# Optimization experiments

Measured on AMD Instinct MI355X. Metric: run time of the kernel, lower is better.

## Reference

```python
import jax, jax.numpy as jnp
import numpy as np

B, S, HOPS, DIM, NREL = 1024, 32, 2, 64, 237
NENT, NEDGE = 14541, 272115
SIGMA = 0.1
CFMW = 64


def setup_inputs() -> dict:
    key = jax.random.key(0)
    ks = jax.random.split(key, 20)

    def g(k, shape):
        return (jax.random.normal(k, shape, dtype=jnp.float32) / np.float32(np.sqrt(shape[0])))

    inp = {
        "entity_pairs": jax.random.randint(ks[0], (B, 2), 0, NENT),
        "train_edges": jax.random.randint(ks[1], (B,), 0, NEDGE),
        "labels": jax.random.randint(ks[2], (B,), 0, NREL),
        "entity2edges": jax.random.randint(ks[3], (NENT + 1, S), 0, NEDGE + 1),
        "edge2entities": jax.random.randint(ks[4], (NEDGE + 1, 1), 0, NENT + 1),
        "edge2relation": jax.random.randint(ks[5], (NEDGE + 1,), 0, NREL + 1),
        "t": jax.random.uniform(ks[6], (B,), dtype=jnp.float32),
        "eps": jax.random.normal(ks[7], (B, NREL), dtype=jnp.float32),
        "rel_feat": g(ks[8], (NREL, DIM)),
        "W_agg0": g(ks[9], (DIM, DIM)), "b_agg0": jnp.zeros((DIM,), jnp.float32),
        "W_agg1": g(ks[10], (DIM, NREL)), "b_agg1": jnp.zeros((NREL,), jnp.float32),
        "W_out": g(ks[11], (2 * NREL, NREL)), "b_out": jnp.zeros((NREL,), jnp.float32),
        "mW1": g(ks[12], (NREL + 1, CFMW)), "mb1": jnp.zeros((CFMW,), jnp.float32),
        "mW2": g(ks[13], (CFMW, CFMW)), "mb2": jnp.zeros((CFMW,), jnp.float32),
        "mW3": g(ks[14], (CFMW, CFMW)), "mb3": jnp.zeros((CFMW,), jnp.float32),
        "mW4": g(ks[15], (CFMW, NREL)), "mb4": jnp.zeros((NREL,), jnp.float32),
    }
    return inp


def _side(ent, labels, train_edges, entity2edges, edge2entities, edge2relation, relf, aggs):
    # multi-hop neighbor edge gather + masks (exclude the training edge itself)
    edges_list = [labels]  # hop-0 "edges" are the relation labels
    masks = []
    for i in range(HOPS):
        if i == 0:
            ne = ent.reshape(B, 1)  # (B, 1) source entities
        else:
            ne = edge2entities[edges_list[-1].reshape(-1)].reshape(B, -1)
        nedges = entity2edges[ne.reshape(-1)].reshape(B, -1)  # (B, S**(i+1))
        edges_list.append(nedges)
        masks.append((nedges != train_edges[:, None]).astype(relf.dtype))
    # edge -> relation -> feature
    ev = [relf[edges_list[0]]]  # (B, DIM)
    for edges in edges_list[1:]:
        ev.append(relf[edge2relation[edges]])  # (B, S**h, DIM)
    # iterative mean aggregation (PathCon-style, one entity per edge)
    for i in range(HOPS):
        W, b, act, self_inc = aggs[i]
        d = W.shape[0]
        nxt = []
        for hop in range(HOPS - i):
            neigh = ev[hop + 1].reshape(B, -1, 1, S, d)
            m = masks[hop].reshape(B, -1, 1, S, 1)
            out = jnp.mean(jnp.mean(neigh * m, axis=-2), axis=-2)  # (B, S**hop, d)
            if self_inc:
                out = out + ev[hop].reshape(B, -1, d)
            nxt.append(act(out @ W + b))
        ev = nxt
    return ev[0].reshape(B, NREL)


def reference(entity_pairs, train_edges, labels, entity2edges, edge2entities,
              edge2relation, t, eps, rel_feat, W_agg0, b_agg0, W_agg1, b_agg1,
              W_out, b_out, mW1, mb1, mW2, mb2, mW3, mb3, mW4, mb4):
    relf = jnp.concatenate([rel_feat, jnp.zeros((1, DIM), rel_feat.dtype)], axis=0)
    aggs = [
        (W_agg0, b_agg0, jax.nn.relu, True),    # intermediate hop: relu, self-included
        (W_agg1, b_agg1, lambda x: x, False),   # last hop: identity, no self
    ]
    x0 = _side(entity_pairs[:, 0], labels, train_edges, entity2edges,
               edge2entities, edge2relation, relf, aggs)
    x1 = _side(entity_pairs[:, 1], labels, train_edges, entity2edges,
               edge2entities, edge2relation, relf, aggs)
    output = jnp.concatenate([x0, x1], axis=-1) @ W_out + b_out  # (B, NREL)
    # CFM: xt = (1-t) x0 + t x1 + sigma*eps ; ut = x1 - x0
    tb = t[:, None]
    xt = (1.0 - tb) * x0 + tb * x1 + SIGMA * eps
    h = jnp.concatenate([xt, tb], axis=-1)
    h = jax.nn.selu(h @ mW1 + mb1)
    h = jax.nn.selu(h @ mW2 + mb2)
    h = jax.nn.selu(h @ mW3 + mb3)
    vt = h @ mW4 + mb4
    scores = output * vt
    return scores
```

## Files before the change

### kernel.cpp

```cpp
#include <hip/hip_runtime.h>
#include <math.h>

#define BB 1024
#define S 32
#define DIM 64
#define NREL 237
#define SIGMA 0.1f

#define OFS_WR    0
#define N_WR      (238*64)
#define OFS_OVEC  (OFS_WR + N_WR)
#define N_OVEC    (2048*64)
#define OFS_WC0   (OFS_OVEC + N_OVEC)
#define N_WC      (64*237)
#define OFS_WC1   (OFS_WC0 + N_WC)
#define OFS_M1    (OFS_WC1 + N_WC)
#define N_M1      (64*64)
#define OFS_BC    (OFS_M1 + N_M1)
#define OFS_HC    (OFS_BC + 237)

__device__ __forceinline__ float selu_f(float x) {
    const float alpha = 1.6732632423543772f;
    const float scale = 1.0507009873554805f;
    return scale * (x > 0.f ? x : alpha * expm1f(x));
}

__global__ __launch_bounds__(256) void precompute_kernel(
    const float* __restrict__ rel_feat, const float* __restrict__ W0,
    const float* __restrict__ W1, const float* __restrict__ b1,
    const float* __restrict__ W_out, const float* __restrict__ b_out,
    const float* __restrict__ mW1, const float* __restrict__ mb1,
    float* __restrict__ ws) {
    __shared__ float red[256];
    int blk = blockIdx.x;
    const int tid = threadIdx.x;

    if (blk < 60) {
        int idx = blk * 256 + tid;
        if (idx < 238 * 64) {
            int r = idx >> 6, o = idx & 63;
            float acc = 0.f;
            if (r < NREL) {
#pragma unroll 8
                for (int d = 0; d < 64; ++d)
                    acc += rel_feat[r * 64 + d] * W0[d * 64 + o];
            }
            ws[OFS_WR + idx] = acc;
        }
        return;
    }
    blk -= 60;
    if (blk < 512) {
        int half = blk >> 8;
        int lb = blk & 255;
        int o = lb >> 2, ct = lb & 3;
        int cl = tid & 63, g = tid >> 6;
        int c = ct * 64 + cl;
        const float* Wsrc = W_out + half * 237 * 237;
        float acc = 0.f;
        if (c < NREL) {
            int k0 = g * 60, k1 = (g == 3) ? 237 : (k0 + 60);
#pragma unroll 4
            for (int k = k0; k < k1; ++k)
                acc += W1[o * 237 + k] * Wsrc[k * 237 + c];
        }
        red[tid] = acc;
        __syncthreads();
        if (g == 0 && c < NREL) {
            float s = red[cl] + red[64 + cl] + red[128 + cl] + red[192 + cl];
            ws[(half ? OFS_WC1 : OFS_WC0) + o * 237 + c] = s;
        }
        return;
    }
    blk -= 512;
    if (blk < 64) {
        int o = blk;
        int w = tid & 63, g = tid >> 6;
        int k0 = g * 60, k1 = (g == 3) ? 237 : (k0 + 60);
        float acc = 0.f;
#pragma unroll 4
        for (int k = k0; k < k1; ++k)
            acc += W1[o * 237 + k] * mW1[k * 64 + w];
        red[tid] = acc;
        __syncthreads();
        if (g == 0)
            ws[OFS_M1 + o * 64 + w] = red[w] + red[64 + w] + red[128 + w] + red[192 + w];
        return;
    }
    blk -= 64;
    if (blk < 4) {
        int cl = tid & 63, g = tid >> 6;
        int c = blk * 64 + cl;
        float acc = 0.f;
        if (c < NREL) {
            int k0 = g * 60, k1 = (g == 3) ? 237 : (k0 + 60);
#pragma unroll 4
            for (int k = k0; k < k1; ++k)
                acc += b1[k] * (W_out[k * 237 + c] + W_out[(237 + k) * 237 + c]);
        }
        red[tid] = acc;
        __syncthreads();
        if (g == 0 && c < NREL)
            ws[OFS_BC + c] = b_out[c] + red[cl] + red[64 + cl] + red[128 + cl] + red[192 + cl];
        return;
    }
    {
        int w = tid & 63, g = tid >> 6;
        int k0 = g * 60, k1 = (g == 3) ? 237 : (k0 + 60);
        float acc = 0.f;
#pragma unroll 4
        for (int k = k0; k < k1; ++k)
            acc += b1[k] * mW1[k * 64 + w];
        red[tid] = acc;
        __syncthreads();
        if (g == 0)
            ws[OFS_HC + w] = mb1[w] + red[w] + red[64 + w] + red[128 + w] + red[192 + w];
    }
}

__global__ __launch_bounds__(256) void gather_kernel(
    const int* __restrict__ ep, const int* __restrict__ te_arr,
    const int* __restrict__ e2e_tab, const int* __restrict__ e2ent,
    const int* __restrict__ e2r, const float* __restrict__ b0,
    float* __restrict__ ws) {
    extern __shared__ float smem[];
    float* s_wr   = smem;
    int*   s_r2m  = (int*)(smem + 15232);
    int*   s_r1   = (int*)(smem + 16256);
    int*   s_ent2 = (int*)(smem + 16288);
    float* s_m1   = smem + 16320;
    float* s_v1   = smem + 16352;

    const int tid = threadIdx.x;
    const int bbase = blockIdx.x * 2;
    const int g = tid >> 4;
    const int c = tid & 15;
    const float4 b0v = ((const float4*)b0)[c];

    {
        const float4* src = (const float4*)(ws + OFS_WR);
        float4* dst = (float4*)s_wr;
        for (int i = tid; i < 238 * 16; i += 256) dst[i] = src[i];
    }
    const float4* sWr4 = (const float4*)s_wr;

    for (int u = 0; u < 4; ++u) {
        const int b = bbase + (u >> 1);
        const int side = u & 1;
        const int te = te_arr[b];
        if (tid < 32) {
            int ent = ep[b * 2 + side];
            int e1 = e2e_tab[ent * S + tid];
            s_r1[tid] = e2r[e1];
            s_m1[tid] = (e1 != te) ? 1.0f : 0.0f;
            s_ent2[tid] = e2ent[e1];
        }
        __syncthreads();
        for (int p = tid; p < 1024; p += 256) {
            int j = p >> 5, s = p & 31;
            int e2 = e2e_tab[s_ent2[j] * S + s];
            s_r2m[p] = (e2 == te) ? NREL : e2r[e2];
        }
        __syncthreads();
        for (int jj = g; jj < 32; jj += 16) {
            float4 acc = sWr4[s_r1[jj] * 16 + c];
            float4 sa = make_float4(0.f, 0.f, 0.f, 0.f);
            float4 sb = make_float4(0.f, 0.f, 0.f, 0.f);
            const int* rr = &s_r2m[jj * 32];
#pragma unroll
            for (int s = 0; s < 16; ++s) {
                float4 v = sWr4[rr[s] * 16 + c];
                sa.x += v.x; sa.y += v.y; sa.z += v.z; sa.w += v.w;
            }
#pragma unroll
            for (int s = 16; s < 32; ++s) {
                float4 v = sWr4[rr[s] * 16 + c];
                sb.x += v.x; sb.y += v.y; sb.z += v.z; sb.w += v.w;
            }
            const float inv = 1.0f / 32.0f;
            float m = s_m1[jj];
            float4 r;
            r.x = fmaxf(acc.x + (sa.x + sb.x) * inv + b0v.x, 0.f) * m;
            r.y = fmaxf(acc.y + (sa.y + sb.y) * inv + b0v.y, 0.f) * m;
            r.z = fmaxf(acc.z + (sa.z + sb.z) * inv + b0v.z, 0.f) * m;
            r.w = fmaxf(acc.w + (sa.w + sb.w) * inv + b0v.w, 0.f) * m;
            *((float4*)&s_v1[jj * 68 + c * 4]) = r;
        }
        __syncthreads();
        if (tid < 64) {
            float sum = 0.f;
#pragma unroll 8
            for (int j = 0; j < 32; ++j) sum += s_v1[j * 68 + tid];
            ws[OFS_OVEC + (b * 2 + side) * 64 + tid] = sum * (1.0f / 32.0f);
        }
        __syncthreads();
    }
}

__global__ __launch_bounds__(256) void final_kernel(
    const float* __restrict__ t_arr, const float* __restrict__ eps,
    const float* __restrict__ mW1, const float* __restrict__ mW2,
    const float* __restrict__ mb2, const float* __restrict__ mW3,
    const float* __restrict__ mb3, const float* __restrict__ mW4,
    const float* __restrict__ mb4, const float* __restrict__ ws,
    float* __restrict__ out) {
    __shared__ float s_o0[2][64], s_o1[2][64], s_omix[2][64];
    __shared__ float s_out[2][240];
    __shared__ float s_red[2][256];
    __shared__ float s_h[2][64];

    const int tid = threadIdx.x;
    const int bb = blockIdx.x * 2;
    const float* ovec = ws + OFS_OVEC;
    const float* Wc0 = ws + OFS_WC0;
    const float* Wc1 = ws + OFS_WC1;
    const float* M1 = ws + OFS_M1;
    const float* bc = ws + OFS_BC;
    const float* hc = ws + OFS_HC;
    const float tb0 = t_arr[bb];
    const float tb1 = t_arr[bb + 1];

    if (tid < 128) {
        int p = tid >> 6, w = tid & 63;
        float tb = p ? tb1 : tb0;
        float o0 = ovec[((bb + p) * 2 + 0) * 64 + w];
        float o1 = ovec[((bb + p) * 2 + 1) * 64 + w];
        s_o0[p][w] = o0; s_o1[p][w] = o1;
        s_omix[p][w] = (1.f - tb) * o0 + tb * o1;
    }
    __syncthreads();

    if (tid < NREL) {
        float a0 = bc[tid], a1 = a0;
#pragma unroll 4
        for (int d = 0; d < 64; ++d) {
            float w0 = Wc0[d * 237 + tid];
            float w1 = Wc1[d * 237 + tid];
            a0 += s_o0[0][d] * w0 + s_o1[0][d] * w1;
            a1 += s_o0[1][d] * w0 + s_o1[1][d] * w1;
        }
        s_out[0][tid] = a0;
        s_out[1][tid] = a1;
    }

    {
        int w = tid & 63, gg = tid >> 6;
        float a0 = 0.f, a1 = 0.f;
        int k0 = gg * 60, k1 = (gg == 3) ? 237 : (k0 + 60);
        const float* e0 = eps + bb * 237;
        const float* e1 = eps + (bb + 1) * 237;
#pragma unroll 4
        for (int k = k0; k < k1; ++k) {
            float m = mW1[k * 64 + w];
            a0 += e0[k] * m;
            a1 += e1[k] * m;
        }
        a0 *= SIGMA; a1 *= SIGMA;
#pragma unroll
        for (int d = gg * 16; d < gg * 16 + 16; ++d) {
            float m = M1[d * 64 + w];
            a0 += s_omix[0][d] * m;
            a1 += s_omix[1][d] * m;
        }
        s_red[0][tid] = a0;
        s_red[1][tid] = a1;
    }
    __syncthreads();
    if (tid < 128) {
        int p = tid >> 6, w = tid & 63;
        float tb = p ? tb1 : tb0;
        float h = hc[w] + tb * mW1[237 * 64 + w]
                + s_red[p][w] + s_red[p][64 + w] + s_red[p][128 + w] + s_red[p][192 + w];
        s_h[p][w] = selu_f(h);
    }
    __syncthreads();

    {
        int w = tid & 63, gg = tid >> 6;
        float a0 = 0.f, a1 = 0.f;
#pragma unroll
        for (int d = gg * 16; d < gg * 16 + 16; ++d) {
            float m = mW2[d * 64 + w];
            a0 += s_h[0][d] * m;
            a1 += s_h[1][d] * m;
        }
        s_red[0][tid] = a0;
        s_red[1][tid] = a1;
    }
    __syncthreads();
    if (tid < 128) {
        int p = tid >> 6, w = tid & 63;
        s_h[p][w] = 0.f;
        float v = mb2[w] + s_red[p][w] + s_red[p][64 + w] + s_red[p][128 + w] + s_red[p][192 + w];
        s_h[p][w] = selu_f(v);
    }
    __syncthreads();

    {
        int w = tid & 63, gg = tid >> 6;
        float a0 = 0.f, a1 = 0.f;
#pragma unroll
        for (int d = gg * 16; d < gg * 16 + 16; ++d) {
            float m = mW3[d * 64 + w];
            a0 += s_h[0][d] * m;
            a1 += s_h[1][d] * m;
        }
        s_red[0][tid] = a0;
        s_red[1][tid] = a1;
    }
    __syncthreads();
    if (tid < 128) {
        int p = tid >> 6, w = tid & 63;
        float v = mb3[w] + s_red[p][w] + s_red[p][64 + w] + s_red[p][128 + w] + s_red[p][192 + w];
        s_h[p][w] = selu_f(v);
    }
    __syncthreads();

    if (tid < NREL) {
        float a0 = mb4[tid], a1 = a0;
#pragma unroll 4
        for (int w = 0; w < 64; ++w) {
            float m = mW4[w * 237 + tid];
            a0 += s_h[0][w] * m;
            a1 += s_h[1][w] * m;
        }
        out[bb * 237 + tid] = s_out[0][tid] * a0;
        out[(bb + 1) * 237 + tid] = s_out[1][tid] * a1;
    }
}

extern "C" void kernel_launch(void* const* d_in, const int* in_sizes, int n_in,
                              void* d_out, int out_size, void* d_ws, size_t ws_size,
                              hipStream_t stream) {
    const int* ep       = (const int*)d_in[0];
    const int* te       = (const int*)d_in[1];
    const int* e2e      = (const int*)d_in[3];
    const int* e2ent    = (const int*)d_in[4];
    const int* e2r      = (const int*)d_in[5];
    const float* t      = (const float*)d_in[6];
    const float* eps    = (const float*)d_in[7];
    const float* relf   = (const float*)d_in[8];
    const float* W0     = (const float*)d_in[9];
    const float* b0     = (const float*)d_in[10];
    const float* W1     = (const float*)d_in[11];
    const float* b1     = (const float*)d_in[12];
    const float* W_out  = (const float*)d_in[13];
    const float* b_out  = (const float*)d_in[14];
    const float* mW1    = (const float*)d_in[15];
    const float* mb1    = (const float*)d_in[16];
    const float* mW2    = (const float*)d_in[17];
    const float* mb2    = (const float*)d_in[18];
    const float* mW3    = (const float*)d_in[19];
    const float* mb3    = (const float*)d_in[20];
    const float* mW4    = (const float*)d_in[21];
    const float* mb4    = (const float*)d_in[22];
    float* ws  = (float*)d_ws;
    float* out = (float*)d_out;

    hipLaunchKernelGGL(precompute_kernel, dim3(641), dim3(256), 0, stream,
                       relf, W0, W1, b1, W_out, b_out, mW1, mb1, ws);
    hipLaunchKernelGGL(gather_kernel, dim3(BB / 2), dim3(256), 74112, stream,
                       ep, te, e2e, e2ent, e2r, b0, ws);
    hipLaunchKernelGGL(final_kernel, dim3(BB / 2), dim3(256), 0, stream,
                       t, eps, mW1, mW2, mb2, mW3, mb3, mW4, mb4, ws, out);
}
```

Measured before the change: 154.8 us.

## Fuse gather and final MLP kernels; compute W1 projection in-kernel instead of precomputed M1

Merges the gather kernel and the final CFM/MLP kernel into one, so the per-pair aggregated vectors stay in shared memory instead of round-tripping through the workspace, and one launch disappears. The precomputed W1·mW1 product (M1) is dropped. Each block now projects the mixed vector through W1 and folds it into the mW1 matvec alongside the noise term. Hop-1 lookups for all four side/pair units are fetched up front, and the next unit's hop-2 indices are prefetched inside the loop. The cost is a larger shared-memory footprint per block and a somewhat bigger matvec per block.

```diff
diff --git a/kernel.cpp b/kernel.cpp
--- a/kernel.cpp
+++ b/kernel.cpp
@@ -9,14 +9,10 @@
 
 #define OFS_WR    0
 #define N_WR      (238*64)
-#define OFS_OVEC  (OFS_WR + N_WR)
-#define N_OVEC    (2048*64)
-#define OFS_WC0   (OFS_OVEC + N_OVEC)
+#define OFS_WC0   (OFS_WR + N_WR)
 #define N_WC      (64*237)
 #define OFS_WC1   (OFS_WC0 + N_WC)
-#define OFS_M1    (OFS_WC1 + N_WC)
-#define N_M1      (64*64)
-#define OFS_BC    (OFS_M1 + N_M1)
+#define OFS_BC    (OFS_WC1 + N_WC)
 #define OFS_HC    (OFS_BC + 237)
 
 __device__ __forceinline__ float selu_f(float x) {
@@ -73,21 +69,6 @@
         return;
     }
     blk -= 512;
-    if (blk < 64) {
-        int o = blk;
-        int w = tid & 63, g = tid >> 6;
-        int k0 = g * 60, k1 = (g == 3) ? 237 : (k0 + 60);
-        float acc = 0.f;
-#pragma unroll 4
-        for (int k = k0; k < k1; ++k)
-            acc += W1[o * 237 + k] * mW1[k * 64 + w];
-        red[tid] = acc;
-        __syncthreads();
-        if (g == 0)
-            ws[OFS_M1 + o * 64 + w] = red[w] + red[64 + w] + red[128 + w] + red[192 + w];
-        return;
-    }
-    blk -= 64;
     if (blk < 4) {
         int cl = tid & 63, g = tid >> 6;
         int c = blk * 64 + cl;
@@ -118,23 +99,31 @@
     }
 }
 
-__global__ __launch_bounds__(256) void gather_kernel(
+__global__ __launch_bounds__(256) void gf_kernel(
     const int* __restrict__ ep, const int* __restrict__ te_arr,
     const int* __restrict__ e2e_tab, const int* __restrict__ e2ent,
     const int* __restrict__ e2r, const float* __restrict__ b0,
-    float* __restrict__ ws) {
+    const float* __restrict__ t_arr, const float* __restrict__ eps,
+    const float* __restrict__ W1, const float* __restrict__ mW1,
+    const float* __restrict__ mW2, const float* __restrict__ mb2,
+    const float* __restrict__ mW3, const float* __restrict__ mb3,
+    const float* __restrict__ mW4, const float* __restrict__ mb4,
+    const float* __restrict__ ws, float* __restrict__ out) {
     extern __shared__ float smem[];
     float* s_wr   = smem;
     int*   s_r2m  = (int*)(smem + 15232);
     int*   s_r1   = (int*)(smem + 16256);
-    int*   s_ent2 = (int*)(smem + 16288);
-    float* s_m1   = smem + 16320;
-    float* s_v1   = smem + 16352;
+    int*   s_ent2 = (int*)(smem + 16384);
+    float* s_m1   = smem + 16512;
+    float* s_v1   = smem + 16640;
+    float* s_ov   = smem + 18816;
 
     const int tid = threadIdx.x;
-    const int bbase = blockIdx.x * 2;
+    const int bb = blockIdx.x * 2;
     const int g = tid >> 4;
     const int c = tid & 15;
+    const int te0 = te_arr[bb];
+    const int te1 = te_arr[bb + 1];
     const float4 b0v = ((const float4*)b0)[c];
 
     {
@@ -144,26 +133,31 @@
     }
     const float4* sWr4 = (const float4*)s_wr;
 
-    for (int u = 0; u < 4; ++u) {
-        const int b = bbase + (u >> 1);
-        const int side = u & 1;
-        const int te = te_arr[b];
-        if (tid < 32) {
-            int ent = ep[b * 2 + side];
-            int e1 = e2e_tab[ent * S + tid];
-            s_r1[tid] = e2r[e1];
-            s_m1[tid] = (e1 != te) ? 1.0f : 0.0f;
-            s_ent2[tid] = e2ent[e1];
-        }
-        __syncthreads();
+    if (tid < 128) {
+        int u = tid >> 5, s = tid & 31;
+        int b = bb + (u >> 1), side = u & 1;
+        int te = (u >> 1) ? te1 : te0;
+        int ent = ep[b * 2 + side];
+        int e1 = e2e_tab[ent * S + s];
+        s_r1[u * 32 + s] = e2r[e1];
+        s_m1[u * 32 + s] = (e1 != te) ? 1.0f : 0.0f;
+        s_ent2[u * 32 + s] = e2ent[e1];
+    }
+    __syncthreads();
+
+    {
+        const int te = te0;
         for (int p = tid; p < 1024; p += 256) {
             int j = p >> 5, s = p & 31;
             int e2 = e2e_tab[s_ent2[j] * S + s];
             s_r2m[p] = (e2 == te) ? NREL : e2r[e2];
         }
-        __syncthreads();
+    }
+    __syncthreads();
+
+    for (int u = 0; u < 4; ++u) {
         for (int jj = g; jj < 32; jj += 16) {
-            float4 acc = sWr4[s_r1[jj] * 16 + c];
+            float4 acc = sWr4[s_r1[u * 32 + jj] * 16 + c];
             float4 sa = make_float4(0.f, 0.f, 0.f, 0.f);
             float4 sb = make_float4(0.f, 0.f, 0.f, 0.f);
             const int* rr = &s_r2m[jj * 32];
@@ -178,7 +172,7 @@
                 sb.x += v.x; sb.y += v.y; sb.z += v.z; sb.w += v.w;
             }
             const float inv = 1.0f / 32.0f;
-            float m = s_m1[jj];
+            float m = s_m1[u * 32 + jj];
             float4 r;
             r.x = fmaxf(acc.x + (sa.x + sb.x) * inv + b0v.x, 0.f) * m;
             r.y = fmaxf(acc.y + (sa.y + sb.y) * inv + b0v.y, 0.f) * m;
@@ -191,57 +185,63 @@
             float sum = 0.f;
 #pragma unroll 8
             for (int j = 0; j < 32; ++j) sum += s_v1[j * 68 + tid];
-            ws[OFS_OVEC + (b * 2 + side) * 64 + tid] = sum * (1.0f / 32.0f);
-        }
-        __syncthreads();
-    }
-}
-
-__global__ __launch_bounds__(256) void final_kernel(
-    const float* __restrict__ t_arr, const float* __restrict__ eps,
-    const float* __restrict__ mW1, const float* __restrict__ mW2,
-    const float* __restrict__ mb2, const float* __restrict__ mW3,
-    const float* __restrict__ mb3, const float* __restrict__ mW4,
-    const float* __restrict__ mb4, const float* __restrict__ ws,
-    float* __restrict__ out) {
-    __shared__ float s_o0[2][64], s_o1[2][64], s_omix[2][64];
-    __shared__ float s_out[2][240];
-    __shared__ float s_red[2][256];
-    __shared__ float s_h[2][64];
-
-    const int tid = threadIdx.x;
-    const int bb = blockIdx.x * 2;
-    const float* ovec = ws + OFS_OVEC;
+            s_ov[u * 64 + tid] = sum * (1.0f / 32.0f);
+        }
+        if (u < 3) {
+            const int un = u + 1;
+            const int te = (un >> 1) ? te1 : te0;
+            for (int p = tid; p < 1024; p += 256) {
+                int j = p >> 5, s = p & 31;
+                int e2 = e2e_tab[s_ent2[un * 32 + j] * S + s];
+                s_r2m[p] = (e2 == te) ? NREL : e2r[e2];
+            }
+        }
+        __syncthreads();
+    }
+
+    float* s_omix = smem;
+    float* s_ymix = smem + 128;
+    float* s_out  = smem + 608;
+    float* s_red  = smem + 1088;
+    float* s_h    = smem + 1600;
+    const float tb0v = t_arr[bb];
+    const float tb1v = t_arr[bb + 1];
     const float* Wc0 = ws + OFS_WC0;
     const float* Wc1 = ws + OFS_WC1;
-    const float* M1 = ws + OFS_M1;
     const float* bc = ws + OFS_BC;
     const float* hc = ws + OFS_HC;
-    const float tb0 = t_arr[bb];
-    const float tb1 = t_arr[bb + 1];
 
     if (tid < 128) {
         int p = tid >> 6, w = tid & 63;
-        float tb = p ? tb1 : tb0;
-        float o0 = ovec[((bb + p) * 2 + 0) * 64 + w];
-        float o1 = ovec[((bb + p) * 2 + 1) * 64 + w];
-        s_o0[p][w] = o0; s_o1[p][w] = o1;
-        s_omix[p][w] = (1.f - tb) * o0 + tb * o1;
+        float tb = p ? tb1v : tb0v;
+        float o0 = s_ov[(p * 2 + 0) * 64 + w];
+        float o1 = s_ov[(p * 2 + 1) * 64 + w];
+        s_omix[p * 64 + w] = (1.f - tb) * o0 + tb * o1;
     }
     __syncthreads();
 
     if (tid < NREL) {
+        float y0 = 0.f, y1 = 0.f;
+#pragma unroll 4
+        for (int d = 0; d < 64; ++d) {
+            float w1v = W1[d * 237 + tid];
+            y0 += s_omix[d] * w1v;
+            y1 += s_omix[64 + d] * w1v;
+        }
+        s_ymix[tid] = y0;
+        s_ymix[240 + tid] = y1;
         float a0 = bc[tid], a1 = a0;
 #pragma unroll 4
         for (int d = 0; d < 64; ++d) {
             float w0 = Wc0[d * 237 + tid];
             float w1 = Wc1[d * 237 + tid];
-            a0 += s_o0[0][d] * w0 + s_o1[0][d] * w1;
-            a1 += s_o0[1][d] * w0 + s_o1[1][d] * w1;
-        }
-        s_out[0][tid] = a0;
-        s_out[1][tid] = a1;
-    }
+            a0 += s_ov[d] * w0 + s_ov[64 + d] * w1;
+            a1 += s_ov[128 + d] * w0 + s_ov[192 + d] * w1;
+        }
+        s_out[tid] = a0;
+        s_out[240 + tid] = a1;
+    }
+    __syncthreads();
 
     {
         int w = tid & 63, gg = tid >> 6;
@@ -252,26 +252,20 @@
 #pragma unroll 4
         for (int k = k0; k < k1; ++k) {
             float m = mW1[k * 64 + w];
-            a0 += e0[k] * m;
-            a1 += e1[k] * m;
-        }
-        a0 *= SIGMA; a1 *= SIGMA;
-#pragma unroll
-        for (int d = gg * 16; d < gg * 16 + 16; ++d) {
-            float m = M1[d * 64 + w];
-            a0 += s_omix[0][d] * m;
-            a1 += s_omix[1][d] * m;
-        }
-        s_red[0][tid] = a0;
-        s_red[1][tid] = a1;
+            a0 += (SIGMA * e0[k] + s_ymix[k]) * m;
+            a1 += (SIGMA * e1[k] + s_ymix[240 + k]) * m;
+        }
+        s_red[tid] = a0;
+        s_red[256 + tid] = a1;
     }
     __syncthreads();
     if (tid < 128) {
         int p = tid >> 6, w = tid & 63;
-        float tb = p ? tb1 : tb0;
+        float tb = p ? tb1v : tb0v;
         float h = hc[w] + tb * mW1[237 * 64 + w]
-                + s_red[p][w] + s_red[p][64 + w] + s_red[p][128 + w] + s_red[p][192 + w];
-        s_h[p][w] = selu_f(h);
+                + s_red[p * 256 + w] + s_red[p * 256 + 64 + w]
+                + s_red[p * 256 + 128 + w] + s_red[p * 256 + 192 + w];
+        s_h[p * 64 + w] = selu_f(h);
     }
     __syncthreads();
 
@@ -281,18 +275,18 @@
 #pragma unroll
         for (int d = gg * 16; d < gg * 16 + 16; ++d) {
             float m = mW2[d * 64 + w];
-            a0 += s_h[0][d] * m;
-            a1 += s_h[1][d] * m;
-        }
-        s_red[0][tid] = a0;
-        s_red[1][tid] = a1;
+            a0 += s_h[d] * m;
+            a1 += s_h[64 + d] * m;
+        }
+        s_red[tid] = a0;
+        s_red[256 + tid] = a1;
     }
     __syncthreads();
     if (tid < 128) {
         int p = tid >> 6, w = tid & 63;
-        s_h[p][w] = 0.f;
-        float v = mb2[w] + s_red[p][w] + s_red[p][64 + w] + s_red[p][128 + w] + s_red[p][192 + w];
-        s_h[p][w] = selu_f(v);
+        float v = mb2[w] + s_red[p * 256 + w] + s_red[p * 256 + 64 + w]
+                + s_red[p * 256 + 128 + w] + s_red[p * 256 + 192 + w];
+        s_h[p * 64 + w] = selu_f(v);
     }
     __syncthreads();
 
@@ -302,17 +296,18 @@
 #pragma unroll
         for (int d = gg * 16; d < gg * 16 + 16; ++d) {
             float m = mW3[d * 64 + w];
-            a0 += s_h[0][d] * m;
-            a1 += s_h[1][d] * m;
-        }
-        s_red[0][tid] = a0;
-        s_red[1][tid] = a1;
+            a0 += s_h[d] * m;
+            a1 += s_h[64 + d] * m;
+        }
+        s_red[tid] = a0;
+        s_red[256 + tid] = a1;
     }
     __syncthreads();
     if (tid < 128) {
         int p = tid >> 6, w = tid & 63;
-        float v = mb3[w] + s_red[p][w] + s_red[p][64 + w] + s_red[p][128 + w] + s_red[p][192 + w];
-        s_h[p][w] = selu_f(v);
+        float v = mb3[w] + s_red[p * 256 + w] + s_red[p * 256 + 64 + w]
+                + s_red[p * 256 + 128 + w] + s_red[p * 256 + 192 + w];
+        s_h[p * 64 + w] = selu_f(v);
     }
     __syncthreads();
 
@@ -321,11 +316,11 @@
 #pragma unroll 4
         for (int w = 0; w < 64; ++w) {
             float m = mW4[w * 237 + tid];
-            a0 += s_h[0][w] * m;
-            a1 += s_h[1][w] * m;
-        }
-        out[bb * 237 + tid] = s_out[0][tid] * a0;
-        out[(bb + 1) * 237 + tid] = s_out[1][tid] * a1;
+            a0 += s_h[w] * m;
+            a1 += s_h[64 + w] * m;
+        }
+        out[bb * 237 + tid] = s_out[tid] * a0;
+        out[(bb + 1) * 237 + tid] = s_out[240 + tid] * a1;
     }
 }
 
@@ -357,10 +352,9 @@
     float* ws  = (float*)d_ws;
     float* out = (float*)d_out;
 
-    hipLaunchKernelGGL(precompute_kernel, dim3(641), dim3(256), 0, stream,
+    hipLaunchKernelGGL(precompute_kernel, dim3(577), dim3(256), 0, stream,
                        relf, W0, W1, b1, W_out, b_out, mW1, mb1, ws);
-    hipLaunchKernelGGL(gather_kernel, dim3(BB / 2), dim3(256), 74112, stream,
-                       ep, te, e2e, e2ent, e2r, b0, ws);
-    hipLaunchKernelGGL(final_kernel, dim3(BB / 2), dim3(256), 0, stream,
-                       t, eps, mW1, mW2, mb2, mW3, mb3, mW4, mb4, ws, out);
+    hipLaunchKernelGGL(gf_kernel, dim3(BB / 2), dim3(256), 76288, stream,
+                       ep, te, e2e, e2ent, e2r, b0,
+                       t, eps, W1, mW1, mW2, mb2, mW3, mb3, mW4, mb4, ws, out);
 }
```

Result: no change. 156.5 us (+1.1%).
